# Kernel optimization log

Measured on AMD Instinct MI355X. Metric: run time of the kernel, lower is better.

Reference implementation:

```python
import jax, jax.numpy as jnp
import numpy as np

# FlowNetC correlation config (matches init_kwargs)
PAD = 20           # pad_size
MAX_DISP = 20      # max_displacement
STRIDE2 = 2        # displacement stride
K = 1              # kernel_size (1x1 patch)
# stride1 = 1, corr_multiply = 1 (multiply mode)

GRID_RAD = MAX_DISP // STRIDE2           # 10
N_DISP = (2 * GRID_RAD + 1) ** 2         # 441 output channels


def _disp_offsets():
    # slice start offsets into the padded input2 for each displacement
    # (dy, dx) in {-GRID_RAD..GRID_RAD} * STRIDE2; start = PAD + d (pad == max_disp)
    d = np.arange(-GRID_RAD, GRID_RAD + 1) * STRIDE2
    dy, dx = np.meshgrid(d, d, indexing='ij')  # row-major: dy outer, dx inner
    return np.stack([PAD + dy.ravel(), PAD + dx.ravel()], axis=1).astype(np.int32)  # [441,2]


def setup_inputs() -> dict:
    key = jax.random.key(0)
    k1, k2 = jax.random.split(key)
    B, C, H, W = 8, 256, 64, 64
    input1 = jax.random.normal(k1, (B, C, H, W), dtype=jnp.float32)
    input2 = jax.random.normal(k2, (B, C, H, W), dtype=jnp.float32)
    return {"input1": input1, "input2": input2}


def reference(input1, input2):
    B, C, H, W = input1.shape
    sumelems = float(K * K * C)  # normalization used by the CUDA kernel
    # zero-pad input2 spatially by PAD (pad_size == max_displacement)
    x2p = jnp.pad(input2, ((0, 0), (0, 0), (PAD, PAD), (PAD, PAD)))
    offs = jnp.asarray(_disp_offsets())  # [441, 2] int32

    def step(carry, off):
        # window of input2 displaced by (dy, dx) relative to input1
        sl = jax.lax.dynamic_slice(x2p, (0, 0, off[0], off[1]), (B, C, H, W))
        corr = jnp.sum(input1 * sl, axis=1) / sumelems  # [B, H, W]
        return carry, corr

    _, out = jax.lax.scan(step, None, offs)       # [441, B, H, W]
    return jnp.transpose(out, (1, 0, 2, 3))       # [B, 441, H, W]
```

## Files before the change

kernel.cpp:

```cpp
#include <hip/hip_runtime.h>
#include <hip/hip_bf16.h>


typedef short    bf16x8 __attribute__((ext_vector_type(8)));
typedef float    f32x4  __attribute__((ext_vector_type(4)));

constexpr int CSTRIDE = 64 * 64;
constexpr int BSTRIDE = 256 * CSTRIDE;

union BF2 { __hip_bfloat162 h; unsigned u; };

__device__ inline unsigned pack_bf2(float lo, float hi) {
    BF2 cv;
    cv.h = __float22bfloat162_rn(make_float2(lo, hi));
    return cv.u;
}

#define ELT(v4, xi) ((xi) == 0 ? (v4).x : (xi) == 1 ? (v4).y : (xi) == 2 ? (v4).z : (v4).w)

__global__ __launch_bounds__(512)
void conv_in2(const float* __restrict__ in2, uint4* __restrict__ out16)
{
    const int tid = threadIdx.x;
    const int b = blockIdx.x & 7;
    const int y = blockIdx.x >> 3;
    const int c8 = tid >> 4;
    const int x0 = (tid & 15) * 4;
    const float* p = in2 + b * BSTRIDE + y * 64 + c8 * 8 * CSTRIDE + x0;
    uint4* dst = out16 + (b * 64 + y) * 2048 + c8 * 64 + x0;

    float4 v[8];
#pragma unroll
    for (int j = 0; j < 8; ++j)
        v[j] = *reinterpret_cast<const float4*>(p + j * CSTRIDE);
#pragma unroll
    for (int xi = 0; xi < 4; ++xi) {
        uint4 o;
        o.x = pack_bf2(ELT(v[0], xi), ELT(v[1], xi));
        o.y = pack_bf2(ELT(v[2], xi), ELT(v[3], xi));
        o.z = pack_bf2(ELT(v[4], xi), ELT(v[5], xi));
        o.w = pack_bf2(ELT(v[6], xi), ELT(v[7], xi));
        dst[xi] = o;
    }
}

__global__ __launch_bounds__(1024, 4)
void corr_mfma(const float* __restrict__ in1,
               const uint4* __restrict__ in2t,
               float* __restrict__ out)
{
    __shared__ float slds[2][2][21 * 65];

    const int tid  = threadIdx.x;
    const int lane = tid & 63;
    const int w    = tid >> 6;
    const int cl   = lane & 15;
    const int q    = lane >> 4;
    const int m    = w & 3;
    const int n    = m + (w >> 2);
    const int b    = blockIdx.x & 7;
    const int p    = blockIdx.x >> 3;
    const int y0   = 4 * (p >> 1) + (p & 1);

    bf16x8 af[2][8];
#pragma unroll
    for (int h = 0; h < 2; ++h) {
        const float* pb = in1 + b * BSTRIDE + (y0 + 2 * h) * 64 + 16 * m + cl
                        + 8 * q * CSTRIDE;
#pragma unroll
        for (int k = 0; k < 8; ++k) {
            const float* pp = pb + 32 * k * CSTRIDE;
            float v[8];
#pragma unroll
            for (int j = 0; j < 8; ++j) v[j] = pp[j * CSTRIDE];
#pragma unroll
            for (int j = 0; j < 4; ++j)
                ((unsigned*)&af[h][k])[j] = pack_bf2(v[2 * j], v[2 * j + 1]);
        }
    }

    const int  x    = 16 * n + cl - 20;
    const bool xok  = (x >= 0) && (x < 64);
    const int  gcol = 16 * n + cl;

    uint4 breg[8];
#pragma unroll
    for (int k = 0; k < 8; ++k) breg[k] = uint4{0u, 0u, 0u, 0u};

    {
        const int yy0 = y0 - 20;
        if (yy0 >= 0 && xok) {
            const uint4* src = in2t + (b * 64 + yy0) * 2048 + q * 64 + x;
#pragma unroll
            for (int k = 0; k < 8; ++k) breg[k] = src[k * 256];
        }
    }

    for (int i = 0; i < 22; ++i) {
        const int  ib      = i & 1;
        const int  yy      = y0 - 20 + 2 * i;
        const bool compute = (yy >= 0) && (yy < 64);

        f32x4 acc0 = {0.f, 0.f, 0.f, 0.f};
        f32x4 acc1 = {0.f, 0.f, 0.f, 0.f};
        if (compute) {
#pragma unroll
            for (int k = 0; k < 8; ++k) {
                const bf16x8 bf = __builtin_bit_cast(bf16x8, breg[k]);
                acc0 = __builtin_amdgcn_mfma_f32_16x16x32_bf16(af[0][k], bf, acc0, 0, 0, 0);
                acc1 = __builtin_amdgcn_mfma_f32_16x16x32_bf16(af[1][k], bf, acc1, 0, 0, 0);
            }
        }

        {
            const int yn = yy + 2;
            if ((i + 1) < 22 && yn >= 0 && yn < 64 && xok) {
                const uint4* src = in2t + (b * 64 + yn) * 2048 + q * 64 + x;
#pragma unroll
                for (int k = 0; k < 8; ++k) breg[k] = src[k * 256];
            }
        }

        if (compute) {
#pragma unroll
            for (int i4 = 0; i4 < 4; ++i4) {
                const int gx = 16 * m + 4 * q + i4;
                const int d2 = gcol - gx;
                if (d2 >= 0 && d2 <= 40 && !(d2 & 1)) {
                    slds[ib][0][(d2 >> 1) * 65 + gx] = acc0[i4];
                    slds[ib][1][(d2 >> 1) * 65 + gx] = acc1[i4];
                }
            }
            __builtin_amdgcn_sched_barrier(0);
            asm volatile("s_waitcnt lgkmcnt(0)" ::: "memory");
            __builtin_amdgcn_s_barrier();
            __builtin_amdgcn_sched_barrier(0);
        }

        const int r0 = i, r1 = i - 1;
#pragma unroll
        for (int t3 = 0; t3 < 3; ++t3) {
            const int t = tid + 1024 * t3;
            if (t < 2 * 21 * 64) {
                const int h  = (t >= 1344) ? 1 : 0;
                const int u  = t - 1344 * h;
                const int dx = u >> 6, gx = u & 63;
                const int r  = h ? r1 : r0;
                if (r >= 0 && r <= 20) {
                    const float val = compute ? slds[ib][h][dx * 65 + gx] * (1.f / 256.f)
                                              : 0.f;
                    out[((b * 441 + r * 21 + dx) * 64 + y0 + 2 * h) * 64 + gx] = val;
                }
            }
        }
    }
}

extern "C" void kernel_launch(void* const* d_in, const int* in_sizes, int n_in,
                              void* d_out, int out_size, void* d_ws, size_t ws_size,
                              hipStream_t stream) {
    const float* in1 = (const float*)d_in[0];
    const float* in2 = (const float*)d_in[1];
    float* out = (float*)d_out;

    conv_in2<<<dim3(512), dim3(512), 0, stream>>>(in2, (uint4*)d_ws);
    corr_mfma<<<dim3(256), dim3(1024), 0, stream>>>(in1, (const uint4*)d_ws, out);
}
```

Before: 181.1 us.

## Stage input2 rows into LDS with async global_load_lds triple buffering

The per-lane register prefetch of input2 rows is replaced by cooperative asynchronous global-to-LDS copies (global_load_lds) into a three-slot row buffer, with the row two steps ahead staged each iteration. Each row is loaded once per block instead of being fetched redundantly by every wave, which cuts global/L2 traffic and register pressure. The cost is extra LDS (about 96KB plus the existing buffers), a full __syncthreads every iteration, and possible ordering hazards because there is no explicit vmcnt wait before the staged data is read. Out-of-range columns now read a shared zero chunk.

Result: faster. 161.7 us (-10.7%).

```diff
diff --git a/kernel.cpp b/kernel.cpp
--- a/kernel.cpp
+++ b/kernel.cpp
@@ -44,12 +44,21 @@
     }
 }
 
+__device__ inline void stage64(const uint4* __restrict__ gsrc, uint4* lds_dst) {
+    __builtin_amdgcn_global_load_lds(
+        (const __attribute__((address_space(1))) void*)gsrc,
+        (__attribute__((address_space(3))) void*)lds_dst,
+        16, 0, 0);
+}
+
 __global__ __launch_bounds__(1024, 4)
 void corr_mfma(const float* __restrict__ in1,
                const uint4* __restrict__ in2t,
                float* __restrict__ out)
 {
+    __shared__ __align__(16) uint4 rowbuf[3][2048];
     __shared__ float slds[2][2][21 * 65];
+    __shared__ __align__(16) uint4 zchunk;
 
     const int tid  = threadIdx.x;
     const int lane = tid & 63;
@@ -61,6 +70,8 @@
     const int b    = blockIdx.x & 7;
     const int p    = blockIdx.x >> 3;
     const int y0   = 4 * (p >> 1) + (p & 1);
+
+    if (tid == 0) { uint4 z = {0u, 0u, 0u, 0u}; zchunk = z; }
 
     bf16x8 af[2][8];
 #pragma unroll
@@ -82,46 +93,42 @@
     const int  x    = 16 * n + cl - 20;
     const bool xok  = (x >= 0) && (x < 64);
     const int  gcol = 16 * n + cl;
-
-    uint4 breg[8];
-#pragma unroll
-    for (int k = 0; k < 8; ++k) breg[k] = uint4{0u, 0u, 0u, 0u};
+    const int  c0   = w * 128 + lane;
 
     {
-        const int yy0 = y0 - 20;
-        if (yy0 >= 0 && xok) {
-            const uint4* src = in2t + (b * 64 + yy0) * 2048 + q * 64 + x;
-#pragma unroll
-            for (int k = 0; k < 8; ++k) breg[k] = src[k * 256];
+        const int yA = y0 - 20;
+        if (yA >= 0 && yA < 64) {
+            const uint4* rp = in2t + (b * 64 + yA) * 2048;
+            stage64(rp + c0,      &rowbuf[0][w * 128]);
+            stage64(rp + c0 + 64, &rowbuf[0][w * 128 + 64]);
+        }
+        const int yB = y0 - 18;
+        if (yB >= 0 && yB < 64) {
+            const uint4* rp = in2t + (b * 64 + yB) * 2048;
+            stage64(rp + c0,      &rowbuf[1][w * 128]);
+            stage64(rp + c0 + 64, &rowbuf[1][w * 128 + 64]);
         }
     }
+    __syncthreads();
+
+    int cur = 0;
 
     for (int i = 0; i < 22; ++i) {
         const int  ib      = i & 1;
         const int  yy      = y0 - 20 + 2 * i;
         const bool compute = (yy >= 0) && (yy < 64);
 
-        f32x4 acc0 = {0.f, 0.f, 0.f, 0.f};
-        f32x4 acc1 = {0.f, 0.f, 0.f, 0.f};
         if (compute) {
+            f32x4 acc0 = {0.f, 0.f, 0.f, 0.f};
+            f32x4 acc1 = {0.f, 0.f, 0.f, 0.f};
+            const uint4* rbase = &rowbuf[cur][q * 64 + x];
 #pragma unroll
             for (int k = 0; k < 8; ++k) {
-                const bf16x8 bf = __builtin_bit_cast(bf16x8, breg[k]);
+                const uint4* pk = xok ? (rbase + k * 256) : &zchunk;
+                const bf16x8 bf = __builtin_bit_cast(bf16x8, *pk);
                 acc0 = __builtin_amdgcn_mfma_f32_16x16x32_bf16(af[0][k], bf, acc0, 0, 0, 0);
                 acc1 = __builtin_amdgcn_mfma_f32_16x16x32_bf16(af[1][k], bf, acc1, 0, 0, 0);
             }
-        }
-
-        {
-            const int yn = yy + 2;
-            if ((i + 1) < 22 && yn >= 0 && yn < 64 && xok) {
-                const uint4* src = in2t + (b * 64 + yn) * 2048 + q * 64 + x;
-#pragma unroll
-                for (int k = 0; k < 8; ++k) breg[k] = src[k * 256];
-            }
-        }
-
-        if (compute) {
 #pragma unroll
             for (int i4 = 0; i4 < 4; ++i4) {
                 const int gx = 16 * m + 4 * q + i4;
@@ -131,10 +138,17 @@
                     slds[ib][1][(d2 >> 1) * 65 + gx] = acc1[i4];
                 }
             }
-            __builtin_amdgcn_sched_barrier(0);
-            asm volatile("s_waitcnt lgkmcnt(0)" ::: "memory");
-            __builtin_amdgcn_s_barrier();
-            __builtin_amdgcn_sched_barrier(0);
+        }
+        __syncthreads();
+
+        {
+            const int yn2 = yy + 4;
+            if (i < 20 && yn2 >= 0 && yn2 < 64) {
+                int nb = cur + 2; if (nb >= 3) nb -= 3;
+                const uint4* rp = in2t + (b * 64 + yn2) * 2048;
+                stage64(rp + c0,      &rowbuf[nb][w * 128]);
+                stage64(rp + c0 + 64, &rowbuf[nb][w * 128 + 64]);
+            }
         }
 
         const int r0 = i, r1 = i - 1;
@@ -153,6 +167,8 @@
                 }
             }
         }
+
+        ++cur; if (cur >= 3) cur = 0;
     }
 }
 
```

## Use per-wave LDS staging to drop block barriers and skip invalid MFMAs

Applied to the files above, without the earlier changes.

Each wave now gets a private LDS tile and writes its own output slice, so the per-iteration block-wide barrier and shared double buffer go away. The register prefetch of the next row of input2 is removed and loads are issued inline per iteration, with a zero dummy address for out-of-range columns. MFMAs for the half-row whose displacement row is out of range are skipped. This trades away the software pipelining of global loads and makes output stores narrower per wave (16-wide segments instead of 64-wide rows), which could hurt store coalescing.

Result: faster. 157.4 us (-13.1%).

```diff
diff --git a/kernel.cpp b/kernel.cpp
--- a/kernel.cpp
+++ b/kernel.cpp
@@ -17,6 +17,8 @@
 }
 
 #define ELT(v4, xi) ((xi) == 0 ? (v4).x : (xi) == 1 ? (v4).y : (xi) == 2 ? (v4).z : (v4).w)
+
+__device__ __align__(16) const uint4 ZERO16 = {0u, 0u, 0u, 0u};
 
 __global__ __launch_bounds__(512)
 void conv_in2(const float* __restrict__ in2, uint4* __restrict__ out16)
@@ -49,7 +51,7 @@
                const uint4* __restrict__ in2t,
                float* __restrict__ out)
 {
-    __shared__ float slds[2][2][21 * 65];
+    __shared__ float slds[16][2][21][17];
 
     const int tid  = threadIdx.x;
     const int lane = tid & 63;
@@ -57,7 +59,8 @@
     const int cl   = lane & 15;
     const int q    = lane >> 4;
     const int m    = w & 3;
-    const int n    = m + (w >> 2);
+    const int d    = w >> 2;
+    const int n    = m + d;
     const int b    = blockIdx.x & 7;
     const int p    = blockIdx.x >> 3;
     const int y0   = 4 * (p >> 1) + (p & 1);
@@ -79,77 +82,73 @@
         }
     }
 
-    const int  x    = 16 * n + cl - 20;
-    const bool xok  = (x >= 0) && (x < 64);
-    const int  gcol = 16 * n + cl;
+    const int  x   = 16 * n + cl - 20;
+    const bool xok = (x >= 0) && (x < 64);
 
-    uint4 breg[8];
-#pragma unroll
-    for (int k = 0; k < 8; ++k) breg[k] = uint4{0u, 0u, 0u, 0u};
+    const int lo_e = (d == 0) ? 0 : 16 * d - 14;
+    const int hi_e = (16 * d + 14 > 40) ? 40 : 16 * d + 14;
+    const int cnt    = ((hi_e - lo_e) >> 1) + 1;
+    const int rounds = (cnt + 3) >> 2;
 
-    {
-        const int yy0 = y0 - 20;
-        if (yy0 >= 0 && xok) {
-            const uint4* src = in2t + (b * 64 + yy0) * 2048 + q * 64 + x;
-#pragma unroll
-            for (int k = 0; k < 8; ++k) breg[k] = src[k * 256];
-        }
-    }
+    float* ms = &slds[w][0][0][0];
+
+    const int s   = lane >> 4;
+    const int pos = lane & 15;
 
     for (int i = 0; i < 22; ++i) {
-        const int  ib      = i & 1;
         const int  yy      = y0 - 20 + 2 * i;
         const bool compute = (yy >= 0) && (yy < 64);
+        const bool h0v     = (i <= 20);
+        const bool h1v     = (i >= 1);
 
-        f32x4 acc0 = {0.f, 0.f, 0.f, 0.f};
-        f32x4 acc1 = {0.f, 0.f, 0.f, 0.f};
         if (compute) {
+            f32x4 acc0 = {0.f, 0.f, 0.f, 0.f};
+            f32x4 acc1 = {0.f, 0.f, 0.f, 0.f};
+            const uint4* src = in2t + (b * 64 + yy) * 2048 + x;
 #pragma unroll
-            for (int k = 0; k < 8; ++k) {
-                const bf16x8 bf = __builtin_bit_cast(bf16x8, breg[k]);
-                acc0 = __builtin_amdgcn_mfma_f32_16x16x32_bf16(af[0][k], bf, acc0, 0, 0, 0);
-                acc1 = __builtin_amdgcn_mfma_f32_16x16x32_bf16(af[1][k], bf, acc1, 0, 0, 0);
+            for (int kb = 0; kb < 2; ++kb) {
+                uint4 wv[4];
+#pragma unroll
+                for (int k4 = 0; k4 < 4; ++k4) {
+                    const int k = kb * 4 + k4;
+                    const uint4* pk = xok ? (src + (4 * k + q) * 64) : &ZERO16;
+                    wv[k4] = *pk;
+                }
+#pragma unroll
+                for (int k4 = 0; k4 < 4; ++k4) {
+                    const int k = kb * 4 + k4;
+                    const bf16x8 bf = __builtin_bit_cast(bf16x8, wv[k4]);
+                    if (h0v) acc0 = __builtin_amdgcn_mfma_f32_16x16x32_bf16(af[0][k], bf, acc0, 0, 0, 0);
+                    if (h1v) acc1 = __builtin_amdgcn_mfma_f32_16x16x32_bf16(af[1][k], bf, acc1, 0, 0, 0);
+                }
+            }
+#pragma unroll
+            for (int i4 = 0; i4 < 4; ++i4) {
+                const int gxl = 4 * q + i4;
+                const int d2  = 16 * d + cl - gxl;
+                if (d2 >= 0 && d2 <= 40 && !(d2 & 1)) {
+                    const int off = (d2 >> 1) * 17 + gxl;
+                    if (h0v) ms[off]       = acc0[i4];
+                    if (h1v) ms[357 + off] = acc1[i4];
+                }
             }
         }
 
-        {
-            const int yn = yy + 2;
-            if ((i + 1) < 22 && yn >= 0 && yn < 64 && xok) {
-                const uint4* src = in2t + (b * 64 + yn) * 2048 + q * 64 + x;
-#pragma unroll
-                for (int k = 0; k < 8; ++k) breg[k] = src[k * 256];
-            }
-        }
-
-        if (compute) {
-#pragma unroll
-            for (int i4 = 0; i4 < 4; ++i4) {
-                const int gx = 16 * m + 4 * q + i4;
-                const int d2 = gcol - gx;
-                if (d2 >= 0 && d2 <= 40 && !(d2 & 1)) {
-                    slds[ib][0][(d2 >> 1) * 65 + gx] = acc0[i4];
-                    slds[ib][1][(d2 >> 1) * 65 + gx] = acc1[i4];
+        for (int rd = 0; rd < rounds; ++rd) {
+            const int d2 = lo_e + 2 * (rd * 4 + s);
+            const int al = (16 * d > d2) ? (16 * d - d2) : 0;
+            int bl = 16 * d + 16 - d2; if (bl > 16) bl = 16;
+            const bool act = (d2 <= hi_e) && (pos >= al) && (pos < bl);
+            if (act) {
+                const int off = (d2 >> 1) * 17 + pos;
+                const int gx  = 16 * m + pos;
+                if (h0v) {
+                    const float v = compute ? ms[off] * (1.f / 256.f) : 0.f;
+                    out[((b * 441 + i * 21 + (d2 >> 1)) * 64 + y0) * 64 + gx] = v;
                 }
-            }
-            __builtin_amdgcn_sched_barrier(0);
-            asm volatile("s_waitcnt lgkmcnt(0)" ::: "memory");
-            __builtin_amdgcn_s_barrier();
-            __builtin_amdgcn_sched_barrier(0);
-        }
-
-        const int r0 = i, r1 = i - 1;
-#pragma unroll
-        for (int t3 = 0; t3 < 3; ++t3) {
-            const int t = tid + 1024 * t3;
-            if (t < 2 * 21 * 64) {
-                const int h  = (t >= 1344) ? 1 : 0;
-                const int u  = t - 1344 * h;
-                const int dx = u >> 6, gx = u & 63;
-                const int r  = h ? r1 : r0;
-                if (r >= 0 && r <= 20) {
-                    const float val = compute ? slds[ib][h][dx * 65 + gx] * (1.f / 256.f)
-                                              : 0.f;
-                    out[((b * 441 + r * 21 + dx) * 64 + y0 + 2 * h) * 64 + gx] = val;
+                if (h1v) {
+                    const float v = compute ? ms[357 + off] * (1.f / 256.f) : 0.f;
+                    out[((b * 441 + (i - 1) * 21 + (d2 >> 1)) * 64 + (y0 + 2)) * 64 + gx] = v;
                 }
             }
         }
```
